# Kernel optimization log

Hardware: AMD Instinct MI355X
Metric: run time of the kernel (lower is better)

The kernel has to match this reference:

```python
import jax, jax.numpy as jnp
import numpy as np

DIM = 32
NUM_FEATURES = 11
N_NODES = 65536
N_EDGES = 262144


def setup_inputs() -> dict:
    key = jax.random.key(0)
    ks = jax.random.split(key, 16)
    s = 0.05
    return {
        "x": jax.random.normal(ks[0], (N_NODES, NUM_FEATURES), dtype=jnp.float32),
        "edge_index": jax.random.randint(ks[1], (2, N_EDGES), 0, N_NODES, dtype=jnp.int32),
        "edge_attr": jax.random.uniform(ks[2], (N_EDGES, 1), dtype=jnp.float32),
        # lin0: num_features -> dim
        "lin0_w": jax.random.normal(ks[3], (NUM_FEATURES, DIM), dtype=jnp.float32) * s,
        "lin0_b": jnp.zeros((DIM,), dtype=jnp.float32),
        # edge MLP: 1 -> 64 -> dim*dim
        "nn_w1": jax.random.normal(ks[4], (1, 64), dtype=jnp.float32) * s,
        "nn_b1": jnp.zeros((64,), dtype=jnp.float32),
        "nn_w2": jax.random.normal(ks[5], (64, DIM * DIM), dtype=jnp.float32) * s,
        "nn_b2": jnp.zeros((DIM * DIM,), dtype=jnp.float32),
        # NNConv root weight + bias
        "root": jax.random.normal(ks[6], (DIM, DIM), dtype=jnp.float32) * s,
        "conv_bias": jnp.zeros((DIM,), dtype=jnp.float32),
        # lin2: dim -> 1
        "lin2_w": jax.random.normal(ks[7], (DIM, 1), dtype=jnp.float32) * s,
        "lin2_b": jnp.zeros((1,), dtype=jnp.float32),
    }


def reference(x, edge_index, edge_attr, lin0_w, lin0_b, nn_w1, nn_b1, nn_w2, nn_b2,
              root, conv_bias, lin2_w, lin2_b):
    N = x.shape[0]
    src, dst = edge_index[0], edge_index[1]

    # out = relu(lin0(x))
    h = jax.nn.relu(x @ lin0_w + lin0_b)  # [N, dim]

    # Per-edge weight matrices from the edge MLP (edge_attr is loop-invariant).
    ew = jax.nn.relu(edge_attr @ nn_w1 + nn_b1) @ nn_w2 + nn_b2  # [E, dim*dim]
    W = ew.reshape(-1, DIM, DIM)  # [E, in, out]

    # In-degree counts for mean aggregation (isolated nodes -> 0, like PyG scatter mean).
    counts = jax.ops.segment_sum(jnp.ones_like(dst, dtype=h.dtype), dst, num_segments=N)
    inv_counts = jnp.where(counts > 0, 1.0 / jnp.maximum(counts, 1.0), 0.0)[:, None]

    def nnconv(h):
        msg = jnp.einsum('ei,eio->eo', h[src], W)  # gather + per-edge matvec
        agg = jax.ops.segment_sum(msg, dst, num_segments=N) * inv_counts  # scatter-mean
        return agg + h @ root + conv_bias

    for _ in range(8):
        h = h + jax.nn.relu(nnconv(h))

    g = jnp.mean(h, axis=0)  # [dim]
    return (g @ lin2_w + lin2_b).reshape(-1)  # [1]
```

## Files before the change

kernel.cpp:

```cpp
#include <hip/hip_runtime.h>

#define N_NODES 65536
#define N_EDGES 262144

typedef _Float16 f16;
typedef __attribute__((ext_vector_type(8))) _Float16 f16x8;
typedef __attribute__((ext_vector_type(4))) float f32x4;


__global__ void prep_kernel(const float* __restrict__ w1, const float* __restrict__ b1,
                            const float* __restrict__ w2, const float* __restrict__ b2,
                            const float* __restrict__ root,
                            f16* __restrict__ Bv16, f16* __restrict__ BvE,
                            f16* __restrict__ Bb16, f16* __restrict__ BbE,
                            f16* __restrict__ Br16, f16* __restrict__ BrE,
                            int* __restrict__ flag) {
    if (blockIdx.x < 4) {
        int jj = blockIdx.x * 256 + threadIdx.x;
        float v = 0.0f, c0 = 0.0f;
#pragma unroll
        for (int k = 0; k < 64; ++k) {
            float w = w1[k];
            if (w > 0.0f) {
                float wv = w2[k * 1024 + jj];
                v += w * wv;
                c0 += b1[k] * wv;
            }
        }
        float bt = c0 + b2[jj];
        int i = jj >> 5, o = jj & 31;
        f16 v16 = (f16)v;
        Bv16[o * 32 + i] = v16;
        BvE[o * 32 + i] = (f16)(v - (float)v16);
        f16 t16 = (f16)bt;
        Bb16[o * 32 + i] = t16;
        BbE[o * 32 + i] = (f16)(bt - (float)t16);
        if (bt != 0.0f) atomicOr(flag, 1);
    } else {
        int jj = (blockIdx.x - 4) * 256 + threadIdx.x;
        int i = jj >> 5, o = jj & 31;
        float r = root[jj];
        f16 r16 = (f16)r;
        Br16[o * 32 + i] = r16;
        BrE[o * 32 + i] = (f16)(r - (float)r16);
    }
}

__global__ void lin0_kernel(const float* __restrict__ x, const float* __restrict__ w,
                            const float* __restrict__ b, f16* __restrict__ h16) {
    int idx = blockIdx.x * 256 + threadIdx.x;
    int n = idx >> 5, j = idx & 31;
    float acc = b[j];
#pragma unroll
    for (int i = 0; i < 11; ++i) acc += x[n * 11 + i] * w[i * 32 + j];
    h16[idx] = (f16)fmaxf(acc, 0.0f);
}

__global__ void hist_kernel(const int* __restrict__ dst, int* __restrict__ counts) {
    int e = blockIdx.x * 256 + threadIdx.x;
    if (e < N_EDGES) atomicAdd(&counts[dst[e]], 1);
}

__global__ void scanA_kernel(const int* __restrict__ counts, int* __restrict__ eoffs,
                             float* __restrict__ inv, int* __restrict__ blockSum) {
    __shared__ int sdata[1024];
    int t = threadIdx.x;
    int gid = blockIdx.x * 1024 + t;
    int c = counts[gid];
    inv[gid] = (c > 0) ? (1.0f / (float)c) : 0.0f;
    sdata[t] = c;
    __syncthreads();
    for (int off = 1; off < 1024; off <<= 1) {
        int v = sdata[t];
        int add = (t >= off) ? sdata[t - off] : 0;
        __syncthreads();
        sdata[t] = v + add;
        __syncthreads();
    }
    eoffs[gid] = sdata[t] - c;
    if (t == 1023) blockSum[blockIdx.x] = sdata[t];
}

__global__ void scanB_kernel(const int* __restrict__ blockSum, int* __restrict__ blockBase,
                             int* __restrict__ offs) {
    if (threadIdx.x == 0) {
        int run = 0;
        for (int b = 0; b < 64; ++b) { blockBase[b] = run; run += blockSum[b]; }
        offs[N_NODES] = run;
    }
}

__global__ void scanC_kernel(const int* __restrict__ eoffs, const int* __restrict__ blockBase,
                             int* __restrict__ offs) {
    int gid = blockIdx.x * 256 + threadIdx.x;
    offs[gid] = eoffs[gid] + blockBase[gid >> 10];
}

__global__ void fill_kernel(const int* __restrict__ src, const int* __restrict__ dst,
                            const float* __restrict__ attr, const int* __restrict__ offs,
                            const float* __restrict__ inv, int* __restrict__ cursor,
                            int2* __restrict__ edgeRec, float* __restrict__ qc) {
    int e = blockIdx.x * 256 + threadIdx.x;
    if (e >= N_EDGES) return;
    int d = dst[e];
    int p = offs[d] + atomicAdd(&cursor[d], 1);
    edgeRec[p] = make_int2((src[e] & 0xffff) | ((d & 3) << 16), __float_as_int(attr[e] * inv[d]));
    qc[p] = inv[d];
}

__global__ __launch_bounds__(256, 4) void iter5_kernel(
    const f16* __restrict__ h16in, f16* __restrict__ h16out,
    const int* __restrict__ offs, const int2* __restrict__ edgeRec,
    const float* __restrict__ qc,
    const f16* __restrict__ Bv16, const f16* __restrict__ BvE,
    const f16* __restrict__ Br16, const f16* __restrict__ BrE,
    const f16* __restrict__ Bb16, const f16* __restrict__ BbE,
    const float* __restrict__ bias, const int* __restrict__ flag) {
    __shared__ float aS[4][16][36];
    __shared__ float bS[4][16][36];
    int t = threadIdx.x;
    int w = t >> 6, lane = t & 63;
    int j = lane & 31, half = lane >> 5;
    int fn = lane & 15, fk = (lane >> 4) * 8;
    bool useB = (flag[0] != 0);
    int g16 = (blockIdx.x * 4 + w) * 16;

    for (int rr = 0; rr < 4; ++rr) {
        int m0 = g16 + rr * 4;
        int pb = offs[m0], pe = offs[m0 + 4];
        float a0 = 0.f, a1 = 0.f, a2 = 0.f, a3 = 0.f;
        int p = pb + half * 8;
        if (p < pe) {
            int2 rc[8];
#pragma unroll
            for (int k = 0; k < 8; ++k) rc[k] = edgeRec[min(p + k, pe - 1)];
            while (true) {
                float g[8];
#pragma unroll
                for (int k = 0; k < 8; ++k) g[k] = (float)h16in[(rc[k].x & 0xffff) * 32 + j];
                int pn = p + 16;
                bool more = (pn < pe);
                int2 rn[8];
                if (more) {
#pragma unroll
                    for (int k = 0; k < 8; ++k) rn[k] = edgeRec[min(pn + k, pe - 1)];
                }
#pragma unroll
                for (int k = 0; k < 8; ++k) {
                    float c = (p + k < pe) ? __int_as_float(rc[k].y) : 0.0f;
                    int dl = (rc[k].x >> 16) & 3;
                    a0 = fmaf((dl == 0) ? c : 0.0f, g[k], a0);
                    a1 = fmaf((dl == 1) ? c : 0.0f, g[k], a1);
                    a2 = fmaf((dl == 2) ? c : 0.0f, g[k], a2);
                    a3 = fmaf((dl == 3) ? c : 0.0f, g[k], a3);
                }
                if (!more) break;
#pragma unroll
                for (int k = 0; k < 8; ++k) rc[k] = rn[k];
                p = pn;
            }
        }
        a0 += __shfl_xor(a0, 32); a1 += __shfl_xor(a1, 32);
        a2 += __shfl_xor(a2, 32); a3 += __shfl_xor(a3, 32);
        aS[w][rr * 4 + 0][j] = a0; aS[w][rr * 4 + 1][j] = a1;
        aS[w][rr * 4 + 2][j] = a2; aS[w][rr * 4 + 3][j] = a3;
        if (useB) {
            float q0 = 0.f, q1 = 0.f, q2 = 0.f, q3 = 0.f;
            for (int pp = pb + half * 8; pp < pe; pp += 16) {
                for (int k = 0; k < 8; ++k) {
                    int idx = min(pp + k, pe - 1);
                    int2 r = edgeRec[idx];
                    float gg = (float)h16in[(r.x & 0xffff) * 32 + j];
                    float c = (pp + k < pe) ? qc[idx] : 0.0f;
                    int dl = (r.x >> 16) & 3;
                    q0 += (dl == 0) ? c * gg : 0.f; q1 += (dl == 1) ? c * gg : 0.f;
                    q2 += (dl == 2) ? c * gg : 0.f; q3 += (dl == 3) ? c * gg : 0.f;
                }
            }
            q0 += __shfl_xor(q0, 32); q1 += __shfl_xor(q1, 32);
            q2 += __shfl_xor(q2, 32); q3 += __shfl_xor(q3, 32);
            bS[w][rr * 4 + 0][j] = q0; bS[w][rr * 4 + 1][j] = q1;
            bS[w][rr * 4 + 2][j] = q2; bS[w][rr * 4 + 3][j] = q3;
        }
    }

    const f16x8 bv0  = *(const f16x8*)&Bv16[fn * 32 + fk];
    const f16x8 bv1  = *(const f16x8*)&Bv16[(fn + 16) * 32 + fk];
    const f16x8 bvE0 = *(const f16x8*)&BvE[fn * 32 + fk];
    const f16x8 bvE1 = *(const f16x8*)&BvE[(fn + 16) * 32 + fk];
    const f16x8 br0  = *(const f16x8*)&Br16[fn * 32 + fk];
    const f16x8 br1  = *(const f16x8*)&Br16[(fn + 16) * 32 + fk];
    const f16x8 brE0 = *(const f16x8*)&BrE[fn * 32 + fk];
    const f16x8 brE1 = *(const f16x8*)&BrE[(fn + 16) * 32 + fk];
    f16x8 a16, aE;
#pragma unroll
    for (int i = 0; i < 8; ++i) {
        float av = aS[w][fn][fk + i];
        f16 lo = (f16)av;
        a16[i] = lo;
        aE[i] = (f16)(av - (float)lo);
    }
    f16x8 hf = *(const f16x8*)&h16in[(g16 + fn) * 32 + fk];
    f32x4 c0 = {0.f, 0.f, 0.f, 0.f}, c1 = {0.f, 0.f, 0.f, 0.f};
    c0 = __builtin_amdgcn_mfma_f32_16x16x32_f16(a16, bv0,  c0, 0, 0, 0);
    c0 = __builtin_amdgcn_mfma_f32_16x16x32_f16(a16, bvE0, c0, 0, 0, 0);
    c0 = __builtin_amdgcn_mfma_f32_16x16x32_f16(aE,  bv0,  c0, 0, 0, 0);
    c0 = __builtin_amdgcn_mfma_f32_16x16x32_f16(hf,  br0,  c0, 0, 0, 0);
    c0 = __builtin_amdgcn_mfma_f32_16x16x32_f16(hf,  brE0, c0, 0, 0, 0);
    c1 = __builtin_amdgcn_mfma_f32_16x16x32_f16(a16, bv1,  c1, 0, 0, 0);
    c1 = __builtin_amdgcn_mfma_f32_16x16x32_f16(a16, bvE1, c1, 0, 0, 0);
    c1 = __builtin_amdgcn_mfma_f32_16x16x32_f16(aE,  bv1,  c1, 0, 0, 0);
    c1 = __builtin_amdgcn_mfma_f32_16x16x32_f16(hf,  br1,  c1, 0, 0, 0);
    c1 = __builtin_amdgcn_mfma_f32_16x16x32_f16(hf,  brE1, c1, 0, 0, 0);
    if (useB) {
        f16x8 ab16, abE;
#pragma unroll
        for (int i = 0; i < 8; ++i) {
            float av = bS[w][fn][fk + i];
            f16 lo = (f16)av;
            ab16[i] = lo;
            abE[i] = (f16)(av - (float)lo);
        }
        f16x8 bb0  = *(const f16x8*)&Bb16[fn * 32 + fk];
        f16x8 bb1  = *(const f16x8*)&Bb16[(fn + 16) * 32 + fk];
        f16x8 bbE0 = *(const f16x8*)&BbE[fn * 32 + fk];
        f16x8 bbE1 = *(const f16x8*)&BbE[(fn + 16) * 32 + fk];
        c0 = __builtin_amdgcn_mfma_f32_16x16x32_f16(ab16, bb0,  c0, 0, 0, 0);
        c0 = __builtin_amdgcn_mfma_f32_16x16x32_f16(ab16, bbE0, c0, 0, 0, 0);
        c0 = __builtin_amdgcn_mfma_f32_16x16x32_f16(abE,  bb0,  c0, 0, 0, 0);
        c1 = __builtin_amdgcn_mfma_f32_16x16x32_f16(ab16, bb1,  c1, 0, 0, 0);
        c1 = __builtin_amdgcn_mfma_f32_16x16x32_f16(ab16, bbE1, c1, 0, 0, 0);
        c1 = __builtin_amdgcn_mfma_f32_16x16x32_f16(abE,  bb1,  c1, 0, 0, 0);
    }

    float bj0 = bias[fn], bj1 = bias[fn + 16];
    int rbase = (lane >> 4) * 4;
#pragma unroll
    for (int r = 0; r < 4; ++r) {
        int n = g16 + rbase + r;
        float hn0 = (float)h16in[n * 32 + fn] + fmaxf(c0[r] + bj0, 0.0f);
        float hn1 = (float)h16in[n * 32 + fn + 16] + fmaxf(c1[r] + bj1, 0.0f);
        h16out[n * 32 + fn] = (f16)hn0;
        h16out[n * 32 + fn + 16] = (f16)hn1;
    }
}


__global__ void reduce_kernel(const f16* __restrict__ h16, float* __restrict__ gacc) {
    int j = threadIdx.x & 31, g = threadIdx.x >> 5;
    float s = 0.0f;
    int node0 = blockIdx.x * 128;
    for (int n = node0 + g; n < node0 + 128; n += 8)
        s += (float)h16[n * 32 + j];
    __shared__ float red[8][32];
    red[g][j] = s;
    __syncthreads();
    if (g == 0) {
        float tt = 0.0f;
        for (int k = 0; k < 8; ++k) tt += red[k][j];
        atomicAdd(&gacc[j], tt);
    }
}

__global__ void out_kernel(const float* __restrict__ gacc, const float* __restrict__ w,
                           const float* __restrict__ b, float* __restrict__ out) {
    if (threadIdx.x == 0) {
        float acc = 0.0f;
        for (int j = 0; j < 32; ++j) acc += gacc[j] * w[j];
        out[0] = acc * (1.0f / (float)N_NODES) + b[0];
    }
}


extern "C" void kernel_launch(void* const* d_in, const int* in_sizes, int n_in,
                              void* d_out, int out_size, void* d_ws, size_t ws_size,
                              hipStream_t stream) {
    (void)in_sizes; (void)n_in; (void)out_size; (void)ws_size;
    const float* x        = (const float*)d_in[0];
    const int*   eidx     = (const int*)d_in[1];
    const float* eattr    = (const float*)d_in[2];
    const float* lin0_w   = (const float*)d_in[3];
    const float* lin0_b   = (const float*)d_in[4];
    const float* nn_w1    = (const float*)d_in[5];
    const float* nn_b1    = (const float*)d_in[6];
    const float* nn_w2    = (const float*)d_in[7];
    const float* nn_b2    = (const float*)d_in[8];
    const float* root     = (const float*)d_in[9];
    const float* conv_b   = (const float*)d_in[10];
    const float* lin2_w   = (const float*)d_in[11];
    const float* lin2_b   = (const float*)d_in[12];
    float* out = (float*)d_out;

    const int* src = eidx;
    const int* dst = eidx + N_EDGES;

    char* ws = (char*)d_ws;
    size_t off = 0;
    f16* h16A = (f16*)(ws + off); off += (size_t)N_NODES * 32 * 2;
    f16* h16B = (f16*)(ws + off); off += (size_t)N_NODES * 32 * 2;
    f16* Bv16 = (f16*)(ws + off); off += 2048;
    f16* BvE  = (f16*)(ws + off); off += 2048;
    f16* Br16 = (f16*)(ws + off); off += 2048;
    f16* BrE  = (f16*)(ws + off); off += 2048;
    f16* Bb16 = (f16*)(ws + off); off += 2048;
    f16* BbE  = (f16*)(ws + off); off += 2048;
    float* inv  = (float*)(ws + off); off += (size_t)N_NODES * 4;
    int*   offs = (int*)(ws + off);   off += 262400;
    int*   eoffs = (int*)(ws + off);  off += (size_t)N_NODES * 4;
    int*   blockSum = (int*)(ws + off);  off += 256;
    int*   blockBase = (int*)(ws + off); off += 256;
    int2*  edgeRec = (int2*)(ws + off); off += (size_t)N_EDGES * 8;
    float* qc   = (float*)(ws + off); off += (size_t)N_EDGES * 4;
    char*  zbase  = ws + off;
    int*   counts = (int*)zbase;
    int*   cursor = (int*)(zbase + (size_t)N_NODES * 4);
    float* gacc   = (float*)(zbase + (size_t)N_NODES * 8);
    int*   flag   = (int*)(zbase + (size_t)N_NODES * 8 + 128);
    size_t zsize  = (size_t)N_NODES * 8 + 256;

    hipMemsetAsync(zbase, 0, zsize, stream);

    prep_kernel<<<8, 256, 0, stream>>>(nn_w1, nn_b1, nn_w2, nn_b2, root,
                                       Bv16, BvE, Bb16, BbE, Br16, BrE, flag);
    lin0_kernel<<<(N_NODES * 32) / 256, 256, 0, stream>>>(x, lin0_w, lin0_b, h16A);
    hist_kernel<<<N_EDGES / 256, 256, 0, stream>>>(dst, counts);
    scanA_kernel<<<N_NODES / 1024, 1024, 0, stream>>>(counts, eoffs, inv, blockSum);
    scanB_kernel<<<1, 64, 0, stream>>>(blockSum, blockBase, offs);
    scanC_kernel<<<N_NODES / 256, 256, 0, stream>>>(eoffs, blockBase, offs);
    fill_kernel<<<N_EDGES / 256, 256, 0, stream>>>(src, dst, eattr, offs, inv, cursor, edgeRec, qc);

    f16* hbuf[2] = {h16A, h16B};
    for (int it = 0; it < 8; ++it) {
        iter5_kernel<<<N_NODES / 64, 256, 0, stream>>>(
            hbuf[it & 1], hbuf[(it + 1) & 1],
            offs, edgeRec, qc, Bv16, BvE, Br16, BrE, Bb16, BbE, conv_b, flag);
    }

    reduce_kernel<<<N_NODES / 128, 256, 0, stream>>>(h16A, gacc);
    out_kernel<<<1, 64, 0, stream>>>(gacc, lin2_w, lin2_b, out);
}
```

Measured before the change: 219.5 us.

## Gather neighbor features from an fp8 copy and fuse final reduction into last iteration

Keeps an fp8 copy of node features alongside the f16 one and uses it for the random neighbor gathers in the edge aggregation, halving the bytes fetched per gathered element. The last iteration no longer writes h and instead accumulates column sums directly into the global accumulator, removing the separate reduce kernel. This adds extra fp8 writes per iteration and loses precision in the aggregated messages, which may hurt accuracy.

```diff
diff --git a/kernel.cpp b/kernel.cpp
--- a/kernel.cpp
+++ b/kernel.cpp
@@ -6,6 +6,15 @@
 typedef _Float16 f16;
 typedef __attribute__((ext_vector_type(8))) _Float16 f16x8;
 typedef __attribute__((ext_vector_type(4))) float f32x4;
+typedef unsigned char u8;
+
+__device__ __forceinline__ u8 enc_fp8(float v) {
+    int p = __builtin_amdgcn_cvt_pk_fp8_f32(v, v, 0, false);
+    return (u8)(p & 0xff);
+}
+__device__ __forceinline__ float dec_fp8(u8 v) {
+    return __builtin_amdgcn_cvt_f32_fp8((int)v, 0);
+}
 
 
 __global__ void prep_kernel(const float* __restrict__ w1, const float* __restrict__ b1,
@@ -47,13 +56,16 @@
 }
 
 __global__ void lin0_kernel(const float* __restrict__ x, const float* __restrict__ w,
-                            const float* __restrict__ b, f16* __restrict__ h16) {
+                            const float* __restrict__ b, f16* __restrict__ h16,
+                            u8* __restrict__ hE8) {
     int idx = blockIdx.x * 256 + threadIdx.x;
     int n = idx >> 5, j = idx & 31;
     float acc = b[j];
 #pragma unroll
     for (int i = 0; i < 11; ++i) acc += x[n * 11 + i] * w[i * 32 + j];
-    h16[idx] = (f16)fmaxf(acc, 0.0f);
+    float hv = fmaxf(acc, 0.0f);
+    h16[idx] = (f16)hv;
+    hE8[idx] = enc_fp8(hv);
 }
 
 __global__ void hist_kernel(const int* __restrict__ dst, int* __restrict__ counts) {
@@ -108,16 +120,19 @@
     qc[p] = inv[d];
 }
 
-__global__ __launch_bounds__(256, 4) void iter5_kernel(
+__global__ __launch_bounds__(256, 4) void iter6_kernel(
     const f16* __restrict__ h16in, f16* __restrict__ h16out,
+    const u8* __restrict__ hE8in, u8* __restrict__ hE8out,
     const int* __restrict__ offs, const int2* __restrict__ edgeRec,
     const float* __restrict__ qc,
     const f16* __restrict__ Bv16, const f16* __restrict__ BvE,
     const f16* __restrict__ Br16, const f16* __restrict__ BrE,
     const f16* __restrict__ Bb16, const f16* __restrict__ BbE,
-    const float* __restrict__ bias, const int* __restrict__ flag) {
+    const float* __restrict__ bias, const int* __restrict__ flag,
+    float* __restrict__ gacc, int last) {
     __shared__ float aS[4][16][36];
     __shared__ float bS[4][16][36];
+    __shared__ float colsum[32];
     int t = threadIdx.x;
     int w = t >> 6, lane = t & 63;
     int j = lane & 31, half = lane >> 5;
@@ -135,9 +150,9 @@
 #pragma unroll
             for (int k = 0; k < 8; ++k) rc[k] = edgeRec[min(p + k, pe - 1)];
             while (true) {
-                float g[8];
-#pragma unroll
-                for (int k = 0; k < 8; ++k) g[k] = (float)h16in[(rc[k].x & 0xffff) * 32 + j];
+                u8 graw[8];
+#pragma unroll
+                for (int k = 0; k < 8; ++k) graw[k] = hE8in[(rc[k].x & 0xffff) * 32 + j];
                 int pn = p + 16;
                 bool more = (pn < pe);
                 int2 rn[8];
@@ -147,12 +162,13 @@
                 }
 #pragma unroll
                 for (int k = 0; k < 8; ++k) {
+                    float g = dec_fp8(graw[k]);
                     float c = (p + k < pe) ? __int_as_float(rc[k].y) : 0.0f;
                     int dl = (rc[k].x >> 16) & 3;
-                    a0 = fmaf((dl == 0) ? c : 0.0f, g[k], a0);
-                    a1 = fmaf((dl == 1) ? c : 0.0f, g[k], a1);
-                    a2 = fmaf((dl == 2) ? c : 0.0f, g[k], a2);
-                    a3 = fmaf((dl == 3) ? c : 0.0f, g[k], a3);
+                    a0 = fmaf((dl == 0) ? c : 0.0f, g, a0);
+                    a1 = fmaf((dl == 1) ? c : 0.0f, g, a1);
+                    a2 = fmaf((dl == 2) ? c : 0.0f, g, a2);
+                    a3 = fmaf((dl == 3) ? c : 0.0f, g, a3);
                 }
                 if (!more) break;
 #pragma unroll
@@ -170,7 +186,7 @@
                 for (int k = 0; k < 8; ++k) {
                     int idx = min(pp + k, pe - 1);
                     int2 r = edgeRec[idx];
-                    float gg = (float)h16in[(r.x & 0xffff) * 32 + j];
+                    float gg = dec_fp8(hE8in[(r.x & 0xffff) * 32 + j]);
                     float c = (pp + k < pe) ? qc[idx] : 0.0f;
                     int dl = (r.x >> 16) & 3;
                     q0 += (dl == 0) ? c * gg : 0.f; q1 += (dl == 1) ? c * gg : 0.f;
@@ -235,30 +251,31 @@
 
     float bj0 = bias[fn], bj1 = bias[fn + 16];
     int rbase = (lane >> 4) * 4;
-#pragma unroll
-    for (int r = 0; r < 4; ++r) {
-        int n = g16 + rbase + r;
-        float hn0 = (float)h16in[n * 32 + fn] + fmaxf(c0[r] + bj0, 0.0f);
-        float hn1 = (float)h16in[n * 32 + fn + 16] + fmaxf(c1[r] + bj1, 0.0f);
-        h16out[n * 32 + fn] = (f16)hn0;
-        h16out[n * 32 + fn + 16] = (f16)hn1;
-    }
-}
-
-
-__global__ void reduce_kernel(const f16* __restrict__ h16, float* __restrict__ gacc) {
-    int j = threadIdx.x & 31, g = threadIdx.x >> 5;
-    float s = 0.0f;
-    int node0 = blockIdx.x * 128;
-    for (int n = node0 + g; n < node0 + 128; n += 8)
-        s += (float)h16[n * 32 + j];
-    __shared__ float red[8][32];
-    red[g][j] = s;
-    __syncthreads();
-    if (g == 0) {
-        float tt = 0.0f;
-        for (int k = 0; k < 8; ++k) tt += red[k][j];
-        atomicAdd(&gacc[j], tt);
+    if (!last) {
+#pragma unroll
+        for (int r = 0; r < 4; ++r) {
+            int n = g16 + rbase + r;
+            float hn0 = (float)h16in[n * 32 + fn] + fmaxf(c0[r] + bj0, 0.0f);
+            float hn1 = (float)h16in[n * 32 + fn + 16] + fmaxf(c1[r] + bj1, 0.0f);
+            h16out[n * 32 + fn] = (f16)hn0;
+            h16out[n * 32 + fn + 16] = (f16)hn1;
+            hE8out[n * 32 + fn] = enc_fp8(hn0);
+            hE8out[n * 32 + fn + 16] = enc_fp8(hn1);
+        }
+    } else {
+        float s0 = 0.0f, s1 = 0.0f;
+#pragma unroll
+        for (int r = 0; r < 4; ++r) {
+            int n = g16 + rbase + r;
+            s0 += (float)h16in[n * 32 + fn] + fmaxf(c0[r] + bj0, 0.0f);
+            s1 += (float)h16in[n * 32 + fn + 16] + fmaxf(c1[r] + bj1, 0.0f);
+        }
+        if (t < 32) colsum[t] = 0.0f;
+        __syncthreads();
+        atomicAdd(&colsum[fn], s0);
+        atomicAdd(&colsum[fn + 16], s1);
+        __syncthreads();
+        if (t < 32) atomicAdd(&gacc[t], colsum[t]);
     }
 }
 
@@ -298,6 +315,8 @@
     size_t off = 0;
     f16* h16A = (f16*)(ws + off); off += (size_t)N_NODES * 32 * 2;
     f16* h16B = (f16*)(ws + off); off += (size_t)N_NODES * 32 * 2;
+    u8*  hE8A = (u8*)(ws + off);  off += (size_t)N_NODES * 32;
+    u8*  hE8B = (u8*)(ws + off);  off += (size_t)N_NODES * 32;
     f16* Bv16 = (f16*)(ws + off); off += 2048;
     f16* BvE  = (f16*)(ws + off); off += 2048;
     f16* Br16 = (f16*)(ws + off); off += 2048;
@@ -322,7 +341,7 @@
 
     prep_kernel<<<8, 256, 0, stream>>>(nn_w1, nn_b1, nn_w2, nn_b2, root,
                                        Bv16, BvE, Bb16, BbE, Br16, BrE, flag);
-    lin0_kernel<<<(N_NODES * 32) / 256, 256, 0, stream>>>(x, lin0_w, lin0_b, h16A);
+    lin0_kernel<<<(N_NODES * 32) / 256, 256, 0, stream>>>(x, lin0_w, lin0_b, h16A, hE8A);
     hist_kernel<<<N_EDGES / 256, 256, 0, stream>>>(dst, counts);
     scanA_kernel<<<N_NODES / 1024, 1024, 0, stream>>>(counts, eoffs, inv, blockSum);
     scanB_kernel<<<1, 64, 0, stream>>>(blockSum, blockBase, offs);
@@ -330,12 +349,13 @@
     fill_kernel<<<N_EDGES / 256, 256, 0, stream>>>(src, dst, eattr, offs, inv, cursor, edgeRec, qc);
 
     f16* hbuf[2] = {h16A, h16B};
+    u8*  ebuf[2] = {hE8A, hE8B};
     for (int it = 0; it < 8; ++it) {
-        iter5_kernel<<<N_NODES / 64, 256, 0, stream>>>(
-            hbuf[it & 1], hbuf[(it + 1) & 1],
-            offs, edgeRec, qc, Bv16, BvE, Br16, BrE, Bb16, BbE, conv_b, flag);
-    }
-
-    reduce_kernel<<<N_NODES / 128, 256, 0, stream>>>(h16A, gacc);
+        iter6_kernel<<<N_NODES / 64, 256, 0, stream>>>(
+            hbuf[it & 1], hbuf[(it + 1) & 1], ebuf[it & 1], ebuf[(it + 1) & 1],
+            offs, edgeRec, qc, Bv16, BvE, Br16, BrE, Bb16, BbE, conv_b, flag,
+            gacc, (it == 7) ? 1 : 0);
+    }
+
     out_kernel<<<1, 64, 0, stream>>>(gacc, lin2_w, lin2_b, out);
 }
```

Result: no change. 217.8 us, median of 2 (-0.8%).
